# Kernel optimization log

Measured on AMD Instinct MI355X. Metric: run time of the kernel, lower is better.

The kernel has to match this reference:

```python
import jax, jax.numpy as jnp
import numpy as np

D_OUT = 1536
BN_EPS = 1e-5


def _batchnorm(h, g, b):
    # torch BatchNorm1d in training mode: biased batch stats
    m = jnp.mean(h, axis=0)
    v = jnp.var(h, axis=0)
    return g * (h - m) * jax.lax.rsqrt(v + BN_EPS) + b


def setup_inputs() -> dict:
    key = jax.random.key(0)
    ks = jax.random.split(key, 16)
    B = 8192
    d0, d1, dib = 1024, 768, 1024
    s = lambda d: (2.0 / d) ** 0.5
    inp = {
        "x0": jax.random.normal(ks[0], (B, d0), jnp.float32),
        "x1": jax.random.normal(ks[1], (B, d1), jnp.float32),
        "x_ib": jax.random.normal(ks[2], (B, dib), jnp.float32),
        # 7 expert projections per source (Reaction_Head_mini modeled as linear proj)
        "pW0": jax.random.normal(ks[3], (7, d0, D_OUT), jnp.float32) * s(d0),
        "pb0": jnp.zeros((7, D_OUT), jnp.float32),
        "pW1": jax.random.normal(ks[4], (7, d1, D_OUT), jnp.float32) * s(d1),
        "pb1": jnp.zeros((7, D_OUT), jnp.float32),
        "pWib": jax.random.normal(ks[5], (7, dib, D_OUT), jnp.float32) * s(dib),
        "pbib": jnp.zeros((7, D_OUT), jnp.float32),
        # MOE_Router_Sig: Linear(1024,512)+BN+relu -> Linear(512,100)+BN+tanh -> Linear(100,3)
        "rw1": jax.random.normal(ks[6], (d0, 512), jnp.float32) * s(d0),
        "rb1": jnp.zeros((512,), jnp.float32),
        "rg1": jnp.ones((512,), jnp.float32),
        "rbt1": jnp.zeros((512,), jnp.float32),
        "rw2": jax.random.normal(ks[7], (512, 100), jnp.float32) * s(512),
        "rb2": jnp.zeros((100,), jnp.float32),
        "rg2": jnp.ones((100,), jnp.float32),
        "rbt2": jnp.zeros((100,), jnp.float32),
        "rw3": jax.random.normal(ks[8], (100, 3), jnp.float32) * s(100),
        "rb3": jnp.zeros((3,), jnp.float32),
    }
    return inp


def reference(x0, x1, x_ib, pW0, pb0, pW1, pb1, pWib, pbib,
              rw1, rb1, rg1, rbt1, rw2, rb2, rg2, rbt2, rw3, rb3):
    # ---- expert projections (torch.no_grad in original) ----
    e0 = jnp.einsum('bd,kdf->bkf', x0, pW0) + pb0      # [B,7,1536]
    e1 = jnp.einsum('bd,kdf->bkf', x1, pW1) + pb1      # [B,7,1536]
    eib = jnp.einsum('bd,kdf->bkf', x_ib, pWib) + pbib # [B,7,1536]
    ex = jnp.concatenate([e0, e1, eib], axis=1)        # [B,21,1536]
    B = ex.shape[0]
    # seg_mean with segment length 7 -> [B,3,1536]
    ex = ex.reshape(B, 3, 7, D_OUT).mean(axis=2)
    ex = jax.lax.stop_gradient(ex)
    # ---- router: MOE_Router_Sig(x0) -> sigmoid -> softmax ----
    h = _batchnorm(x0 @ rw1 + rb1, rg1, rbt1)
    h = jax.nn.relu(h)
    h = _batchnorm(h @ rw2 + rb2, rg2, rbt2)
    h = jnp.tanh(h)
    logits = jax.nn.sigmoid(h @ rw3 + rb3)             # [B,3]
    w = jax.nn.softmax(logits, axis=-1)                # [B,3]
    # ---- weighted combine + L2 normalize ----
    out = jnp.sum(ex * w[:, :, None], axis=1)          # [B,1536]
    out = out / jnp.linalg.norm(out, axis=-1, keepdims=True).clip(1e-12)
    return out
```

## Files before the change

kernel.cpp:

```cpp
#include <hip/hip_runtime.h>
#include <stdint.h>

typedef __attribute__((ext_vector_type(8))) short short8;
typedef __attribute__((ext_vector_type(4))) float floatx4;

__device__ inline unsigned short f2bf(float f) {
    unsigned int u = __float_as_uint(f);
    u += 0x7fffu + ((u >> 16) & 1u);
    return (unsigned short)(u >> 16);
}

__device__ void avg_transpose_tile(const float* __restrict__ src,
                                   unsigned short* __restrict__ dst,
                                   int E, int K, int Nsrc, int Ndst, int ldb,
                                   float scale, int tile_x, int tile_y) {
    __shared__ float tile[32][33];
    const int tid = threadIdx.x;
    const int tx = tid & 31;
    const int ty = tid >> 5;
    const int kb = tile_x * 32;
    const int nb = tile_y * 32;
#pragma unroll
    for (int p = 0; p < 4; ++p) {
        int kl = ty + p * 8;
        int k = kb + kl;
        int n = nb + tx;
        float s = 0.f;
        if (k < K && n < Nsrc) {
            for (int e = 0; e < E; ++e)
                s += src[(size_t)e * K * Nsrc + (size_t)k * Nsrc + n];
        }
        tile[kl][tx] = s * scale;
    }
    __syncthreads();
#pragma unroll
    for (int p = 0; p < 4; ++p) {
        int nl = ty + p * 8;
        int n = nb + nl;
        int k = kb + tx;
        if (n < Ndst && k < K)
            dst[(size_t)n * ldb + k] = f2bf(tile[tx][nl]);
    }
}

__global__ __launch_bounds__(256) void prep(
    const float* __restrict__ pW0, const float* __restrict__ pW1,
    const float* __restrict__ pWib, const float* __restrict__ rw1,
    const float* __restrict__ rw2, const float* __restrict__ pb0,
    const float* __restrict__ pb1, const float* __restrict__ pbib,
    const float* __restrict__ x0,
    unsigned short* __restrict__ Wmt, unsigned short* __restrict__ rw1t,
    unsigned short* __restrict__ rw2t, float* __restrict__ bm0,
    float* __restrict__ bm1, float* __restrict__ bm2,
    float* __restrict__ stats_zero, unsigned short* __restrict__ X0b) {
    int id = blockIdx.x;
    int tid = threadIdx.x;
    if (id < 1536) {
        avg_transpose_tile(pW0, Wmt + 0, 7, 1024, 1536, 1536, 2816, 1.f / 7.f,
                           id % 32, id / 32);
    } else if (id < 2688) {
        int t = id - 1536;
        avg_transpose_tile(pW1, Wmt + 1024, 7, 768, 1536, 1536, 2816, 1.f / 7.f,
                           t % 24, t / 24);
    } else if (id < 4224) {
        int t = id - 2688;
        avg_transpose_tile(pWib, Wmt + 1792, 7, 1024, 1536, 1536, 2816,
                           1.f / 7.f, t % 32, t / 32);
    } else if (id < 4736) {
        int t = id - 4224;
        avg_transpose_tile(rw1, rw1t, 1, 1024, 512, 512, 1024, 1.f, t % 32,
                           t / 32);
    } else if (id < 4800) {
        int t = id - 4736;
        avg_transpose_tile(rw2, rw2t, 1, 512, 100, 128, 512, 1.f, t % 16,
                           t / 16);
    } else if (id < 4806) {
        int i = (id - 4800) * 256 + tid;
        if (i < 1536) {
            float s0 = 0.f, s1 = 0.f, s2 = 0.f;
            for (int e = 0; e < 7; ++e) {
                s0 += pb0[e * 1536 + i];
                s1 += pb1[e * 1536 + i];
                s2 += pbib[e * 1536 + i];
            }
            const float inv = 1.f / 7.f;
            bm0[i] = s0 * inv; bm1[i] = s1 * inv; bm2[i] = s2 * inv;
        }
    } else if (id < 4807) {
        for (int i = tid; i < 1280; i += 256) stats_zero[i] = 0.f;
    } else {
        int base = (id - 4807) * 1024;
#pragma unroll
        for (int k = 0; k < 4; ++k) {
            int i = base + k * 256 + tid;
            float4 v = ((const float4*)x0)[i];
            ushort4 o;
            o.x = f2bf(v.x); o.y = f2bf(v.y); o.z = f2bf(v.z); o.w = f2bf(v.w);
            ((ushort4*)X0b)[i] = o;
        }
    }
}

template <int MODE>
__global__ __launch_bounds__(256) void gemm_bt(
    const unsigned short* __restrict__ A, const unsigned short* __restrict__ Bt,
    float* __restrict__ C, int K, int Nreal, int ldc,
    const float* __restrict__ bias, float* __restrict__ sum,
    float* __restrict__ sumsq, const float* __restrict__ w0,
    const float* __restrict__ w1, const float* __restrict__ w2,
    const float* __restrict__ bm0, const float* __restrict__ bm1,
    const float* __restrict__ bm2) {
    __shared__ __align__(16) unsigned short As[128 * 32];
    __shared__ __align__(16) unsigned short Bs[128 * 32];
    const int tid = threadIdx.x;
    const int lane = tid & 63;
    const int wv = tid >> 6;
    const int bm_off = blockIdx.x * 128;
    const int bn_off = blockIdx.y * 128;
    const int wm = (wv & 1) * 64;
    const int wn = (wv >> 1) * 64;
    floatx4 acc[4][4];
#pragma unroll
    for (int i = 0; i < 4; ++i)
#pragma unroll
        for (int j = 0; j < 4; ++j) acc[i][j] = (floatx4){0.f, 0.f, 0.f, 0.f};

    const int quad = lane >> 4;
    const int lrow = lane & 15;
    const int srow = lane >> 2;
    const int scol = (lane & 3) * 8;

    const unsigned short* Ag = A + (size_t)bm_off * K;
    const unsigned short* Bg = Bt + (size_t)bn_off * K;

    for (int k0 = 0; k0 < K; k0 += 32) {
#pragma unroll
        for (int r = 0; r < 2; ++r) {
            int chunk = r * 4 + wv;
            {
                const unsigned short* gp =
                    Ag + (size_t)(chunk * 16 + srow) * K + (k0 + scol);
                __builtin_amdgcn_global_load_lds(
                    (const __attribute__((address_space(1))) void*)gp,
                    (__attribute__((address_space(3))) void*)(As + chunk * 512),
                    16, 0, 0);
            }
            {
                const unsigned short* gp =
                    Bg + (size_t)(chunk * 16 + srow) * K + (k0 + scol);
                __builtin_amdgcn_global_load_lds(
                    (const __attribute__((address_space(1))) void*)gp,
                    (__attribute__((address_space(3))) void*)(Bs + chunk * 512),
                    16, 0, 0);
            }
        }
        __syncthreads();
        short8 af[4], bfr[4];
#pragma unroll
        for (int i = 0; i < 4; ++i)
            af[i] = *(const short8*)(As + (wm + i * 16 + lrow) * 32 + quad * 8);
#pragma unroll
        for (int j = 0; j < 4; ++j)
            bfr[j] = *(const short8*)(Bs + (wn + j * 16 + lrow) * 32 + quad * 8);
#pragma unroll
        for (int i = 0; i < 4; ++i)
#pragma unroll
            for (int j = 0; j < 4; ++j)
                acc[i][j] = __builtin_amdgcn_mfma_f32_16x16x32_bf16(
                    af[i], bfr[j], acc[i][j], 0, 0, 0);
        __syncthreads();
    }

    if (MODE == 1) {
#pragma unroll
        for (int i = 0; i < 4; ++i) {
#pragma unroll
            for (int r = 0; r < 4; ++r) {
                int m = bm_off + wm + i * 16 + quad * 4 + r;
                float wb0 = w0[m], wb1 = w1[m], wb2 = w2[m];
#pragma unroll
                for (int j = 0; j < 4; ++j) {
                    int n = bn_off + wn + j * 16 + lrow;
                    float v = acc[i][j][r] + wb0 * bm0[n] + wb1 * bm1[n] +
                              wb2 * bm2[n];
                    C[(size_t)m * ldc + n] = v;
                }
            }
        }
    } else {
#pragma unroll
        for (int j = 0; j < 4; ++j) {
            int n = bn_off + wn + j * 16 + lrow;
            bool nok = (n < Nreal);
            float bv = nok ? bias[n] : 0.f;
            float s = 0.f, ss = 0.f;
#pragma unroll
            for (int i = 0; i < 4; ++i) {
#pragma unroll
                for (int r = 0; r < 4; ++r) {
                    float v = acc[i][j][r] + bv;
                    int m = bm_off + wm + i * 16 + quad * 4 + r;
                    if (nok) C[(size_t)m * ldc + n] = v;
                    s += v; ss += v * v;
                }
            }
            s += __shfl_xor(s, 16); s += __shfl_xor(s, 32);
            ss += __shfl_xor(ss, 16); ss += __shfl_xor(ss, 32);
            if (quad == 0 && nok) {
                atomicAdd(&sum[n], s);
                atomicAdd(&sumsq[n], ss);
            }
        }
    }
}

__global__ __launch_bounds__(256) void bn_relu_pack(
    const float* __restrict__ h, unsigned short* __restrict__ out,
    const float* __restrict__ sum, const float* __restrict__ sumsq,
    const float* __restrict__ g, const float* __restrict__ b) {
    __shared__ float sc[512], sh[512];
    const float invB = 1.f / 8192.f;
    for (int c = threadIdx.x; c < 512; c += 256) {
        float m = sum[c] * invB;
        float v = sumsq[c] * invB - m * m;
        float s = g[c] * rsqrtf(v + 1e-5f);
        sc[c] = s;
        sh[c] = b[c] - m * s;
    }
    __syncthreads();
    int base = blockIdx.x * 4096;
#pragma unroll
    for (int k = 0; k < 16; ++k) {
        int i = base + k * 256 + threadIdx.x;
        int c4 = (i & 127) * 4;
        float4 v = ((const float4*)h)[i];
        ushort4 o;
        o.x = f2bf(fmaxf(v.x * sc[c4 + 0] + sh[c4 + 0], 0.f));
        o.y = f2bf(fmaxf(v.y * sc[c4 + 1] + sh[c4 + 1], 0.f));
        o.z = f2bf(fmaxf(v.z * sc[c4 + 2] + sh[c4 + 2], 0.f));
        o.w = f2bf(fmaxf(v.w * sc[c4 + 3] + sh[c4 + 3], 0.f));
        ((ushort4*)out)[i] = o;
    }
}

__global__ __launch_bounds__(128) void router_tail(
    const float* __restrict__ h2, const float* __restrict__ sum,
    const float* __restrict__ sumsq, const float* __restrict__ g,
    const float* __restrict__ b, const float* __restrict__ rw3,
    const float* __restrict__ rb3, float* __restrict__ w0,
    float* __restrict__ w1, float* __restrict__ w2) {
    __shared__ float sc[100], sh[100], w3[300], b3[3];
    int tid = threadIdx.x;
    const float invB = 1.f / 8192.f;
    if (tid < 100) {
        float m = sum[tid] * invB;
        float v = sumsq[tid] * invB - m * m;
        float s = g[tid] * rsqrtf(v + 1e-5f);
        sc[tid] = s;
        sh[tid] = b[tid] - m * s;
    }
    for (int i = tid; i < 300; i += 128) w3[i] = rw3[i];
    if (tid < 3) b3[tid] = rb3[tid];
    __syncthreads();
    int bi = blockIdx.x * 128 + tid;
    float l0 = b3[0], l1 = b3[1], l2 = b3[2];
    const float* hr = h2 + (size_t)bi * 100;
    for (int k = 0; k < 100; ++k) {
        float t = tanhf(hr[k] * sc[k] + sh[k]);
        l0 += t * w3[k * 3 + 0];
        l1 += t * w3[k * 3 + 1];
        l2 += t * w3[k * 3 + 2];
    }
    l0 = 1.f / (1.f + expf(-l0));
    l1 = 1.f / (1.f + expf(-l1));
    l2 = 1.f / (1.f + expf(-l2));
    float mx = fmaxf(l0, fmaxf(l1, l2));
    float e0 = expf(l0 - mx), e1 = expf(l1 - mx), e2 = expf(l2 - mx);
    float inv = 1.f / (e0 + e1 + e2);
    w0[bi] = e0 * inv; w1[bi] = e1 * inv; w2[bi] = e2 * inv;
}

__global__ __launch_bounds__(256) void pack_xp(
    const float* __restrict__ x0, const float* __restrict__ x1,
    const float* __restrict__ xib, const float* __restrict__ w0,
    const float* __restrict__ w1, const float* __restrict__ w2,
    unsigned short* __restrict__ Xp) {
    int i = blockIdx.x * blockDim.x + threadIdx.x;
    if (i >= 8192 * 704) return;
    int b = i / 704;
    int g = i % 704;
    const float* src;
    float w;
    int col;
    if (g < 256)      { src = x0 + (size_t)b * 1024 + g * 4;          w = w0[b]; col = g * 4; }
    else if (g < 448) { src = x1 + (size_t)b * 768 + (g - 256) * 4;   w = w1[b]; col = 1024 + (g - 256) * 4; }
    else              { src = xib + (size_t)b * 1024 + (g - 448) * 4; w = w2[b]; col = 1792 + (g - 448) * 4; }
    float4 v = *(const float4*)src;
    ushort4 o;
    o.x = f2bf(v.x * w); o.y = f2bf(v.y * w);
    o.z = f2bf(v.z * w); o.w = f2bf(v.w * w);
    *(ushort4*)(Xp + (size_t)b * 2816 + col) = o;
}

__global__ __launch_bounds__(256) void l2norm_rows(float* __restrict__ out) {
    int wv = threadIdx.x >> 6;
    int lane = threadIdx.x & 63;
    int row = blockIdx.x * 4 + wv;
    float4* rp = (float4*)(out + (size_t)row * 1536);
    float4 v[6];
    float ss = 0.f;
#pragma unroll
    for (int t = 0; t < 6; ++t) {
        v[t] = rp[lane + t * 64];
        ss += v[t].x * v[t].x + v[t].y * v[t].y + v[t].z * v[t].z + v[t].w * v[t].w;
    }
#pragma unroll
    for (int o = 32; o > 0; o >>= 1) ss += __shfl_xor(ss, o);
    float inv = 1.f / fmaxf(sqrtf(ss), 1e-12f);
#pragma unroll
    for (int t = 0; t < 6; ++t) {
        v[t].x *= inv; v[t].y *= inv; v[t].z *= inv; v[t].w *= inv;
        rp[lane + t * 64] = v[t];
    }
}

extern "C" void kernel_launch(void* const* d_in, const int* in_sizes, int n_in,
                              void* d_out, int out_size, void* d_ws,
                              size_t ws_size, hipStream_t stream) {
    (void)in_sizes; (void)n_in; (void)out_size; (void)ws_size;
    const float* x0   = (const float*)d_in[0];
    const float* x1   = (const float*)d_in[1];
    const float* xib  = (const float*)d_in[2];
    const float* pW0  = (const float*)d_in[3];
    const float* pb0  = (const float*)d_in[4];
    const float* pW1  = (const float*)d_in[5];
    const float* pb1  = (const float*)d_in[6];
    const float* pWib = (const float*)d_in[7];
    const float* pbib = (const float*)d_in[8];
    const float* rw1  = (const float*)d_in[9];
    const float* rb1  = (const float*)d_in[10];
    const float* rg1  = (const float*)d_in[11];
    const float* rbt1 = (const float*)d_in[12];
    const float* rw2  = (const float*)d_in[13];
    const float* rb2  = (const float*)d_in[14];
    const float* rg2  = (const float*)d_in[15];
    const float* rbt2 = (const float*)d_in[16];
    const float* rw3  = (const float*)d_in[17];
    const float* rb3  = (const float*)d_in[18];
    float* out = (float*)d_out;

    char* ws = (char*)d_ws;
    unsigned short* Wmt = (unsigned short*)(ws);
    char* stats = ws + 8650752;
    float* sum1   = (float*)(stats + 0);
    float* sumsq1 = (float*)(stats + 2048);
    float* sum2   = (float*)(stats + 4096);
    float* sumsq2 = (float*)(stats + 4608);
    float* bm0    = (float*)(stats + 10240);
    float* bm1    = (float*)(stats + 16384);
    float* bm2    = (float*)(stats + 22528);
    float* w0p    = (float*)(stats + 28672);
    float* w1p    = (float*)(stats + 61440);
    float* w2p    = (float*)(stats + 94208);
    unsigned short* rw1t = (unsigned short*)(ws + 8781824);
    unsigned short* rw2t = (unsigned short*)(ws + 9830400);
    char* R5 = ws + 9961472;
    unsigned short* X0b = (unsigned short*)(R5);
    float* h1           = (float*)(R5 + 16777216);
    unsigned short* h1n = (unsigned short*)(R5 + 33554432);
    float* h2           = (float*)(R5 + 41943040);
    unsigned short* Xp  = (unsigned short*)(R5);

    prep<<<6855, 256, 0, stream>>>(pW0, pW1, pWib, rw1, rw2, pb0, pb1, pbib, x0,
                                   Wmt, rw1t, rw2t, bm0, bm1, bm2,
                                   (float*)stats, X0b);
    gemm_bt<2><<<dim3(64, 4), 256, 0, stream>>>(
        X0b, rw1t, h1, 1024, 512, 512, rb1, sum1, sumsq1,
        nullptr, nullptr, nullptr, nullptr, nullptr, nullptr);
    bn_relu_pack<<<256, 256, 0, stream>>>(h1, h1n, sum1, sumsq1, rg1, rbt1);
    gemm_bt<2><<<dim3(64, 1), 256, 0, stream>>>(
        h1n, rw2t, h2, 512, 100, 100, rb2, sum2, sumsq2,
        nullptr, nullptr, nullptr, nullptr, nullptr, nullptr);
    router_tail<<<64, 128, 0, stream>>>(h2, sum2, sumsq2, rg2, rbt2, rw3, rb3,
                                        w0p, w1p, w2p);
    pack_xp<<<22528, 256, 0, stream>>>(x0, x1, xib, w0p, w1p, w2p, Xp);
    gemm_bt<1><<<dim3(64, 12), 256, 0, stream>>>(
        Xp, Wmt, out, 2816, 1536, 1536, nullptr, nullptr, nullptr,
        w0p, w1p, w2p, bm0, bm1, bm2);
    l2norm_rows<<<2048, 256, 0, stream>>>(out);
}
```

Before: 483.8 us.

## Replace main combine GEMM with 256x192-tile direct-to-LDS pipelined kernel

Adds a new GEMM kernel for the main weighted-expert projection. Each block computes a 256x192 tile with 8 waves, loads A and B into a 4-stage LDS ring through global_load_lds with XOR swizzling, and uses explicit vmcnt waits and setprio around the MFMA bursts. It also switches to a grid swizzle of 256 blocks. The aim is more operand reuse per block and better overlap of global loads with MFMA work than the previous 64x12-grid gemm_bt. In exchange it adds hand-tuned waitcnt counts and uses a large LDS footprint, which limits occupancy.

After: 421.7 us. -12.8%, faster.

```diff
diff --git a/kernel.cpp b/kernel.cpp
--- a/kernel.cpp
+++ b/kernel.cpp
@@ -214,6 +214,169 @@
     }
 }
 
+__global__ __launch_bounds__(512, 2) void gemm256(
+    const unsigned short* __restrict__ A, const unsigned short* __restrict__ Bt,
+    float* __restrict__ C, int K, int ldc,
+    const float* __restrict__ w0, const float* __restrict__ w1,
+    const float* __restrict__ w2, const float* __restrict__ g0,
+    const float* __restrict__ g1, const float* __restrict__ g2) {
+    __shared__ __align__(16) unsigned short lds[57344];
+    unsigned short* Asb = lds;
+    unsigned short* Bsb = lds + 32768;
+
+    const int tid = threadIdx.x;
+    const int lane = tid & 63;
+    const int wv = tid >> 6;
+    const int wm = wv >> 2;
+    const int wn = wv & 3;
+    const int quad = lane >> 4;
+    const int lrow = lane & 15;
+
+    int id = blockIdx.y * 32 + blockIdx.x;
+    id = (id & 7) * 32 + (id >> 3);
+    const int row0 = (id & 31) * 256;
+    const int col0 = (id >> 5) * 192;
+
+    size_t srcA[2];
+#pragma unroll
+    for (int c = 0; c < 2; ++c) {
+        int idx = c * 512 + tid;
+        int r = idx >> 2;
+        int sl = (idx & 3) ^ ((r >> 1) & 3);
+        srcA[c] = (size_t)(row0 + r) * K + sl * 8;
+    }
+    size_t srcB16;
+    {
+        int r = tid >> 2;
+        int sl = (tid & 3) ^ ((r >> 1) & 3);
+        srcB16 = (size_t)(col0 + r) * K + sl * 8;
+    }
+    size_t srcB4[2];
+#pragma unroll
+    for (int d = 0; d < 2; ++d) {
+        int byteoff = d * 2048 + tid * 4;
+        int r = 128 + (byteoff >> 6);
+        int sl = ((byteoff >> 4) & 3) ^ ((r >> 1) & 3);
+        srcB4[d] = (size_t)(col0 + r) * K + sl * 8 + ((tid & 3) << 1);
+    }
+
+    auto stageA = [&](int kt, int buf) {
+        const int k0 = kt * 32;
+#pragma unroll
+        for (int c = 0; c < 2; ++c) {
+            __builtin_amdgcn_global_load_lds(
+                (const __attribute__((address_space(1))) void*)(A + srcA[c] + k0),
+                (__attribute__((address_space(3))) void*)(Asb + buf * 8192 +
+                                                         c * 4096 + wv * 512),
+                16, 0, 0);
+        }
+    };
+    auto stageB = [&](int kt, int buf) {
+        const int k0 = kt * 32;
+        __builtin_amdgcn_global_load_lds(
+            (const __attribute__((address_space(1))) void*)(Bt + srcB16 + k0),
+            (__attribute__((address_space(3))) void*)(Bsb + buf * 6144 +
+                                                     wv * 512),
+            16, 0, 0);
+#pragma unroll
+        for (int d = 0; d < 2; ++d) {
+            __builtin_amdgcn_global_load_lds(
+                (const __attribute__((address_space(1))) void*)(Bt + srcB4[d] + k0),
+                (__attribute__((address_space(3))) void*)(Bsb + buf * 6144 +
+                                                         4096 + d * 1024 +
+                                                         wv * 128),
+                4, 0, 0);
+        }
+    };
+
+    floatx4 acc[8][3];
+#pragma unroll
+    for (int i = 0; i < 8; ++i)
+#pragma unroll
+        for (int j = 0; j < 3; ++j) acc[i][j] = (floatx4){0.f, 0.f, 0.f, 0.f};
+
+    const int NT = K >> 5;
+    stageA(0, 0); stageB(0, 0);
+    stageA(1, 1); stageB(1, 1);
+    stageA(2, 2); stageB(2, 2);
+    asm volatile("s_waitcnt vmcnt(10)" ::: "memory");
+    asm volatile("s_barrier" ::: "memory");
+
+    for (int t = 0; t < NT; ++t) {
+        const int buf = t & 3;
+        const int nb = (t + 3) & 3;
+        const bool pre = (t + 3 < NT);
+        const unsigned short* Ab = Asb + buf * 8192;
+        const unsigned short* Bb = Bsb + buf * 6144;
+
+        if (pre) stageA(t + 3, nb);
+        short8 bfr[3];
+#pragma unroll
+        for (int j = 0; j < 3; ++j) {
+            int r = wn * 48 + j * 16 + lrow;
+            bfr[j] = *(const short8*)(Bb + r * 32 +
+                                      ((quad ^ ((r >> 1) & 3)) << 3));
+        }
+        short8 af0[4];
+#pragma unroll
+        for (int i = 0; i < 4; ++i) {
+            int r = wm * 128 + i * 16 + lrow;
+            af0[i] = *(const short8*)(Ab + r * 32 +
+                                      ((quad ^ ((r >> 1) & 3)) << 3));
+        }
+        __builtin_amdgcn_s_setprio(1);
+#pragma unroll
+        for (int i = 0; i < 4; ++i)
+#pragma unroll
+            for (int j = 0; j < 3; ++j)
+                acc[i][j] = __builtin_amdgcn_mfma_f32_16x16x32_bf16(
+                    af0[i], bfr[j], acc[i][j], 0, 0, 0);
+        __builtin_amdgcn_s_setprio(0);
+
+        if (pre) stageB(t + 3, nb);
+        short8 af1[4];
+#pragma unroll
+        for (int i = 0; i < 4; ++i) {
+            int r = wm * 128 + 64 + i * 16 + lrow;
+            af1[i] = *(const short8*)(Ab + r * 32 +
+                                      ((quad ^ ((r >> 1) & 3)) << 3));
+        }
+        __builtin_amdgcn_s_setprio(1);
+#pragma unroll
+        for (int i = 0; i < 4; ++i)
+#pragma unroll
+            for (int j = 0; j < 3; ++j)
+                acc[4 + i][j] = __builtin_amdgcn_mfma_f32_16x16x32_bf16(
+                    af1[i], bfr[j], acc[4 + i][j], 0, 0, 0);
+        __builtin_amdgcn_s_setprio(0);
+
+        if (t + 1 < NT) {
+            if (t + 3 < NT)
+                asm volatile("s_waitcnt vmcnt(10)" ::: "memory");
+            else if (t + 2 < NT)
+                asm volatile("s_waitcnt vmcnt(5)" ::: "memory");
+            else
+                asm volatile("s_waitcnt vmcnt(0)" ::: "memory");
+            asm volatile("s_barrier" ::: "memory");
+        }
+    }
+
+#pragma unroll
+    for (int ii = 0; ii < 8; ++ii) {
+#pragma unroll
+        for (int r = 0; r < 4; ++r) {
+            int m = row0 + wm * 128 + ii * 16 + quad * 4 + r;
+            float a0 = w0[m], a1 = w1[m], a2 = w2[m];
+#pragma unroll
+            for (int j = 0; j < 3; ++j) {
+                int n = col0 + wn * 48 + j * 16 + lrow;
+                C[(size_t)m * ldc + n] =
+                    acc[ii][j][r] + a0 * g0[n] + a1 * g1[n] + a2 * g2[n];
+            }
+        }
+    }
+}
+
 __global__ __launch_bounds__(256) void bn_relu_pack(
     const float* __restrict__ h, unsigned short* __restrict__ out,
     const float* __restrict__ sum, const float* __restrict__ sumsq,
@@ -384,8 +547,7 @@
     router_tail<<<64, 128, 0, stream>>>(h2, sum2, sumsq2, rg2, rbt2, rw3, rb3,
                                         w0p, w1p, w2p);
     pack_xp<<<22528, 256, 0, stream>>>(x0, x1, xib, w0p, w1p, w2p, Xp);
-    gemm_bt<1><<<dim3(64, 12), 256, 0, stream>>>(
-        Xp, Wmt, out, 2816, 1536, 1536, nullptr, nullptr, nullptr,
-        w0p, w1p, w2p, bm0, bm1, bm2);
+    gemm256<<<dim3(32, 8), 512, 0, stream>>>(Xp, Wmt, out, 2816, 1536,
+                                             w0p, w1p, w2p, bm0, bm1, bm2);
     l2norm_rows<<<2048, 256, 0, stream>>>(out);
 }
```
